# Optimization experiments

Measured on AMD Instinct MI355X. Metric: run time of the kernel, lower is better.

The kernel has to match this reference:

```python
import jax, jax.numpy as jnp
import numpy as np
from jax import lax

B, H, W, C = 8, 128, 128, 256
HEADS, WIN, PRETRAIN = 8, 8, 8
QK_U = C // HEADS            # 32
QK_CH = QK_U * HEADS         # 256
KV_CH = QK_CH + C            # 512
BLOCK = WIN // 2             # key block size at half resolution
HALO = WIN                   # halo window (halo_window//2) at half resolution
PAD = (HALO - BLOCK) // 2    # halo overlap pad at half resolution


def _win_part(x, heads):
    b, h, w, c = x.shape
    u = c // heads
    x = x.reshape(b, h // WIN, WIN, w // WIN, WIN, heads, u)
    x = x.transpose(0, 1, 3, 5, 2, 4, 6)
    return x.reshape(b, (h // WIN) * (w // WIN), heads, WIN * WIN, u)


def _halo_part(x):
    # overlapping halo blocks: [b,hh,wh,c] -> [b, nw, HALO*HALO, c]
    b, h, w, c = x.shape
    xp = jnp.pad(x, ((0, 0), (PAD, PAD), (PAD, PAD), (0, 0)))
    hb, wb = h // BLOCK, w // BLOCK
    ih = jnp.arange(hb)[:, None] * BLOCK + jnp.arange(HALO)[None, :]
    iw = jnp.arange(wb)[:, None] * BLOCK + jnp.arange(HALO)[None, :]
    t = xp[:, ih][:, :, :, iw]            # [b, hb, HALO, wb, HALO, c]
    t = t.transpose(0, 1, 3, 2, 4, 5)
    return t.reshape(b, hb * wb, HALO * HALO, c)


def _halo_part_fused(x, heads):
    t = _halo_part(x)
    b, nw, l, c = t.shape
    u = c // heads
    return t.reshape(b, nw, l, heads, u).transpose(0, 1, 3, 2, 4)


def _l2n(x):
    # tf.math.l2_normalize with epsilon=1.55e-5
    return x * lax.rsqrt(jnp.maximum(jnp.sum(x * x, -1, keepdims=True), 1.55e-5))


def _rel_bias(cpb_w1, cpb_b1, cpb_w2):
    # Swin-V2 style continuous (log-CPB) relative bias between full-res query
    # window and half-res halo key window.
    qc = jnp.arange(WIN, dtype=jnp.float32)
    kc = (jnp.arange(HALO, dtype=jnp.float32) - PAD) * 2.0 + 0.5  # half-res centers in full-res coords
    r1 = qc[:, None] - kc[None, :]
    rel_y = jnp.broadcast_to(r1[:, None, :, None], (WIN, WIN, HALO, HALO))
    rel_x = jnp.broadcast_to(r1[None, :, None, :], (WIN, WIN, HALO, HALO))
    rel = jnp.stack([rel_y, rel_x], -1).reshape(WIN * WIN, HALO * HALO, 2)
    rel = rel / (PRETRAIN - 1) * 8.0
    rel = jnp.sign(rel) * jnp.log2(jnp.abs(rel) + 1.0) / np.float32(np.log2(8.0))
    hmid = jax.nn.relu(rel @ cpb_w1 + cpb_b1)
    bias = 16.0 * jax.nn.sigmoid(hmid @ cpb_w2)   # [q, k, heads]
    return bias.transpose(2, 0, 1)[None, None]    # [1,1,heads,q,k]


def _pad_mask(dtype):
    # No outer divisible-pad here (H,W divisible), but halo zero-padding at the
    # image border must be masked out (-100 on out-of-image key positions).
    m = jnp.ones((1, H // 2, W // 2, 1), dtype)   # min-pooled validity map (all ones)
    hm = _halo_part(m)                            # [1, nw, HALO*HALO, 1]; border halos -> 0
    return -100.0 * (hm[..., 0] == 0).astype(dtype)[:, :, None, None, :]  # [1,nw,1,1,k]


def reference(inputs, qkv_w, q_bias, v_bias, dw_w, dw_gamma, dw_beta, dw_mean, dw_var, scale, cpb_w1, cpb_b1, cpb_w2, proj_w, proj_b):
    qkv = jnp.einsum('bhwc,cd->bhwd', inputs, qkv_w)
    q, kv = qkv[..., :QK_CH], qkv[..., QK_CH:]
    # depthwise 3x3 stride-2 conv + (inference) batch-norm on K/V path
    kv = lax.conv_general_dilated(kv, dw_w, (2, 2), 'SAME',
                                  dimension_numbers=('NHWC', 'HWIO', 'NHWC'),
                                  feature_group_count=KV_CH)
    kv = (kv - dw_mean) * lax.rsqrt(dw_var + 1e-3) * dw_gamma + dw_beta
    q = q + q_bias
    kv = kv + jnp.concatenate([jnp.zeros_like(q_bias), v_bias])
    qw = _win_part(q, HEADS)                                 # [B,nw,h,64,QK_U]
    k = _halo_part_fused(kv[..., :QK_CH], HEADS)             # [B,nw,h,64,QK_U]
    v = _halo_part_fused(kv[..., QK_CH:], HEADS)             # [B,nw,h,64,V_U]
    logit_scale = jnp.exp(jnp.minimum(scale, np.float32(np.log(100.0))))  # [h,1,1]
    attn = jnp.einsum('bnhqd,bnhkd->bnhqk', _l2n(qw) * logit_scale, _l2n(k))
    attn = attn + _rel_bias(cpb_w1, cpb_b1, cpb_w2) + _pad_mask(attn.dtype)
    attn = jax.nn.softmax(attn, axis=-1)
    out = jnp.einsum('bnhqk,bnhkd->bnhqd', attn, v)
    hb, wb = H // WIN, W // WIN
    out = out.reshape(B, hb, wb, HEADS, WIN, WIN, C // HEADS)
    out = out.transpose(0, 1, 4, 2, 5, 3, 6).reshape(B, H, W, C)
    return jnp.einsum('bhwc,cd->bhwd', out, proj_w) + proj_b


def setup_inputs() -> dict:
    key = jax.random.key(0)
    ks = jax.random.split(key, 16)
    rn = lambda k, s, sc=0.05: jax.random.normal(k, s, jnp.float32) * sc
    return {
        'inputs': jax.random.normal(ks[0], (B, H, W, C), jnp.float32),
        'qkv_w': rn(ks[1], (C, 2 * QK_CH + C)),
        'q_bias': rn(ks[2], (QK_CH,)),
        'v_bias': rn(ks[3], (C,)),
        'dw_w': rn(ks[4], (3, 3, 1, KV_CH)),
        'dw_gamma': 1.0 + rn(ks[5], (KV_CH,)),
        'dw_beta': rn(ks[6], (KV_CH,)),
        'dw_mean': rn(ks[7], (KV_CH,)),
        'dw_var': jax.random.uniform(ks[8], (KV_CH,), jnp.float32, 0.5, 1.5),
        'scale': jnp.full((HEADS, 1, 1), np.log(10.0), jnp.float32),
        'cpb_w1': rn(ks[9], (2, 512), 0.5),
        'cpb_b1': rn(ks[10], (512,), 0.1),
        'cpb_w2': rn(ks[11], (512, HEADS), 0.1),
        'proj_w': rn(ks[12], (C, C)),
        'proj_b': rn(ks[13], (C,)),
    }
```

## Files before the change

kernel.cpp:

```cpp
#include <hip/hip_runtime.h>
#include <stdint.h>


typedef __attribute__((ext_vector_type(8))) short short8;
typedef __attribute__((ext_vector_type(4))) short short4v;
typedef __attribute__((ext_vector_type(4))) float f32x4;

#define VT_PLANE 4624L

__device__ __forceinline__ float bf2f(unsigned short u){
  union { unsigned int i; float f; } x; x.i = ((unsigned int)u)<<16; return x.f;
}
__device__ __forceinline__ unsigned short f2bf(float f){
  union { float f; unsigned int i; } x; x.f = f;
  unsigned int r = x.i + 0x7FFFu + ((x.i>>16)&1u);
  return (unsigned short)(r>>16);
}
__device__ __forceinline__ unsigned int pack_bf_t(float a, float b){
  union { float f; unsigned int u; } x, y; x.f = a; y.f = b;
  return (y.u & 0xFFFF0000u) | (x.u >> 16);
}
__device__ __forceinline__ void gl_lds16(const void* g, void* l){
  __builtin_amdgcn_global_load_lds((const __attribute__((address_space(1))) unsigned int*)g,
                                   (__attribute__((address_space(3))) unsigned int*)l, 16, 0, 0);
}

__global__ __launch_bounds__(256) void cvt_bf16_kernel(const float* __restrict__ in,
                                                       short* __restrict__ out, long n8)
{
  long stride = (long)gridDim.x * 256;
  for (long i = (long)blockIdx.x*256 + threadIdx.x; i < n8; i += stride){
    float4 a = ((const float4*)in)[2*i];
    float4 b = ((const float4*)in)[2*i+1];
    short8 v;
    v[0]=(short)f2bf(a.x); v[1]=(short)f2bf(a.y); v[2]=(short)f2bf(a.z); v[3]=(short)f2bf(a.w);
    v[4]=(short)f2bf(b.x); v[5]=(short)f2bf(b.y); v[6]=(short)f2bf(b.z); v[7]=(short)f2bf(b.w);
    ((short8*)out)[i] = v;
  }
}

__global__ void transpose_w_kernel(const float* __restrict__ w, short* __restrict__ wt,
                                   int K, int N)
{
  int idx = blockIdx.x*256 + threadIdx.x;
  if (idx >= K*N) return;
  int n = idx / K, k = idx - n*K;
  wt[idx] = (short)f2bf(w[(long)k*N + n]);
}

__global__ __launch_bounds__(64) void relbias_kernel(const float* __restrict__ w1,
    const float* __restrict__ b1, const float* __restrict__ w2, float* __restrict__ out)
{
  int q = blockIdx.x;
  int k = threadIdx.x;
  float ry = (float)(q>>3) - (((float)(k>>3) - 2.f)*2.f + 0.5f);
  float rx = (float)(q&7)  - (((float)(k&7)  - 2.f)*2.f + 0.5f);
  ry *= (8.f/7.f); rx *= (8.f/7.f);
  float sy = (ry>0.f)?1.f:((ry<0.f)?-1.f:0.f);
  float sx = (rx>0.f)?1.f:((rx<0.f)?-1.f:0.f);
  ry = sy * log2f(fabsf(ry)+1.f) * (1.f/3.f);
  rx = sx * log2f(fabsf(rx)+1.f) * (1.f/3.f);
  float acc[8] = {0,0,0,0,0,0,0,0};
  for (int j=0;j<512;j++){
    float hm = ry*w1[j] + rx*w1[512+j] + b1[j];
    hm = fmaxf(hm, 0.f);
#pragma unroll
    for (int h=0;h<8;h++) acc[h] += hm * w2[j*8+h];
  }
#pragma unroll
  for (int h=0;h<8;h++)
    out[h*4096 + q*64 + k] = (16.f / (1.f + __expf(-acc[h]))) * 1.4426950408889634f;
}

template<int ND, int OUTMODE, int MTILES>
__global__ __launch_bounds__(256) void gemm_bt_kernel(const short* __restrict__ A,
    const short* __restrict__ Bt, const float* __restrict__ bias,
    short* __restrict__ out_q, short* __restrict__ out_kv, float* __restrict__ out_f)
{
  __shared__ short smem[32768];
  const int tid  = threadIdx.x;
  const int lane = tid & 63;
  const int wid  = tid >> 6;
  const int wr = wid >> 1, wc = wid & 1;
  const int g = lane >> 4, q15 = lane & 15;

  constexpr int NCB = ND / 128;
  constexpr int NSUP_X = (1024 / MTILES) / 8;
  const int bid = blockIdx.x;
  const int xcd = bid & 7;
  const int idx = bid >> 3;
  const int sup = xcd * NSUP_X + idx / NCB;
  const long row0 = (long)sup * (128 * MTILES);
  const int  col0 = (idx % NCB) * 128;

  f32x4 acc[4][4];
#pragma unroll
  for (int m=0;m<4;m++)
#pragma unroll
    for (int n=0;n<4;n++) acc[m][n] = (f32x4){0.f,0.f,0.f,0.f};

  auto stage = [&](int s){
    int buf = s & 1;
    long rowt = row0 + (long)(s >> 2) * 128;
    int kt = (s & 3) * 64;
#pragma unroll
    for (int j = 0; j < 4; j++) {
      int f = j*256 + tid;
      int r = f >> 3, p = f & 7;
      gl_lds16(A + (rowt + r)*256 + kt + ((p ^ (r&7))<<3),
               smem + buf*16384 + ((j*256 + (wid<<6))<<3));
      gl_lds16(Bt + (long)(col0 + r)*256 + kt + ((p ^ (r&7))<<3),
               smem + buf*16384 + 8192 + ((j*256 + (wid<<6))<<3));
    }
  };
  auto compute = [&](int buf){
    const short* As = smem + buf*16384;
    const short* Bs = As + 8192;
#pragma unroll
    for (int ks = 0; ks < 2; ks++) {
      short8 af[4], bfv[4];
#pragma unroll
      for (int m=0;m<4;m++){
        int r = wr*64 + m*16 + q15;
        int gg = ks*4 + g;
        af[m] = *(const short8*)(As + r*64 + ((gg ^ (r&7))<<3));
      }
#pragma unroll
      for (int n=0;n<4;n++){
        int r = wc*64 + n*16 + q15;
        int gg = ks*4 + g;
        bfv[n] = *(const short8*)(Bs + r*64 + ((gg ^ (r&7))<<3));
      }
#pragma unroll
      for (int m=0;m<4;m++)
#pragma unroll
        for (int n=0;n<4;n++)
          acc[m][n] = __builtin_amdgcn_mfma_f32_16x16x32_bf16(af[m], bfv[n], acc[m][n], 0, 0, 0);
    }
  };

  stage(0);
  __syncthreads();

  for (int t = 0; t < MTILES; t++){
#pragma unroll
    for (int k = 0; k < 4; k++){
      int s = t*4 + k;
      if (s + 1 < MTILES*4) stage(s+1);
      compute(s & 1);
      __syncthreads();
    }

    if (OUTMODE == 0) {
      short* sc = smem + 16384;
#pragma unroll
      for (int m=0;m<4;m++){
#pragma unroll
        for (int n=0;n<4;n++){
          int col = wc*64 + n*16 + q15;
          int cg = col >> 3;
          float bv = (col0 + col < 256) ? bias[col0 + col] : 0.f;
#pragma unroll
          for (int rg=0;rg<4;rg++){
            int row = wr*64 + m*16 + g*4 + rg;
            sc[row*128 + ((cg ^ (row&7))<<3) + (col&7)] = (short)f2bf(acc[m][n][rg] + bv);
          }
        }
      }
      __syncthreads();
      {
        int row = tid >> 1, ch = tid & 1;
        long grow = row0 + (long)t*128 + row;
#pragma unroll
        for (int j=0;j<8;j++){
          int cg = ch*8 + j;
          short8 v = *(const short8*)(sc + row*128 + ((cg ^ (row&7))<<3));
          int col = col0 + cg*8;
          if (col0 < 256) *(short8*)(out_q + grow*256 + col)        = v;
          else            *(short8*)(out_kv + grow*512 + (col-256)) = v;
        }
      }
      __syncthreads();
    } else {
      float* fsc = (float*)(smem + 16384);
#pragma unroll
      for (int p=0;p<2;p++){
        if (wr == p){
#pragma unroll
          for (int m=0;m<4;m++){
#pragma unroll
            for (int n=0;n<4;n++){
              int col = wc*64 + n*16 + q15;
              int c4 = col >> 2;
              float bv = bias[col0 + col];
#pragma unroll
              for (int rg=0;rg<4;rg++){
                int rl = m*16 + g*4 + rg;
                fsc[rl*128 + ((c4 ^ (rl&7))<<2) + (col&3)] = acc[m][n][rg] + bv;
              }
            }
          }
        }
        __syncthreads();
        {
          int rl = tid >> 2;
          long grow = row0 + (long)t*128 + p*64 + rl;
#pragma unroll
          for (int j=0;j<8;j++){
            int c4 = (tid&3)*8 + j;
            float4 v = *(const float4*)(fsc + rl*128 + ((c4 ^ (rl&7))<<2));
            *(float4*)(out_f + grow*ND + col0 + c4*4) = v;
          }
        }
        __syncthreads();
      }
    }
#pragma unroll
    for (int m=0;m<4;m++)
#pragma unroll
      for (int n=0;n<4;n++) acc[m][n] = (f32x4){0.f,0.f,0.f,0.f};
  }
}

__global__ __launch_bounds__(256) void dwconv_kernel(const short* __restrict__ kv_buf,
    const float* __restrict__ dw_w, const float* __restrict__ gamma,
    const float* __restrict__ beta, const float* __restrict__ mean,
    const float* __restrict__ var, const float* __restrict__ v_bias,
    short* __restrict__ kv_K, short* __restrict__ v_t)
{
  __shared__ short vls[32][256];

  const int bid = blockIdx.x;
  const int b  = bid >> 7;
  const int rem = bid & 127;
  const int y2 = rem >> 1, xq = rem & 1;
  const int tid = threadIdx.x;
  const int lane = tid & 63, w = tid >> 6;
  const int ch0 = lane * 8;

  float s[8], sh[8];
#pragma unroll
  for (int i=0;i<8;i+=4){
    float4 g4 = *(const float4*)(gamma + ch0 + i);
    float4 v4 = *(const float4*)(var   + ch0 + i);
    float4 m4 = *(const float4*)(mean  + ch0 + i);
    float4 b4 = *(const float4*)(beta  + ch0 + i);
    float gg[4] = {g4.x,g4.y,g4.z,g4.w}, vv[4] = {v4.x,v4.y,v4.z,v4.w};
    float mm[4] = {m4.x,m4.y,m4.z,m4.w}, bb[4] = {b4.x,b4.y,b4.z,b4.w};
#pragma unroll
    for (int j=0;j<4;j++){
      float sv = gg[j] * rsqrtf(vv[j] + 1e-3f);
      s[i+j]  = sv;
      sh[i+j] = bb[j] - mm[j]*sv;
    }
  }
  if (ch0 >= 256){
    float4 vb0 = *(const float4*)(v_bias + ch0 - 256);
    float4 vb1 = *(const float4*)(v_bias + ch0 - 252);
    sh[0]+=vb0.x; sh[1]+=vb0.y; sh[2]+=vb0.z; sh[3]+=vb0.w;
    sh[4]+=vb1.x; sh[5]+=vb1.y; sh[6]+=vb1.z; sh[7]+=vb1.w;
  }

  float wv[9][8];
#pragma unroll
  for (int t=0;t<9;t++){
    float4 w0 = *(const float4*)(dw_w + t*512 + ch0);
    float4 w1 = *(const float4*)(dw_w + t*512 + ch0 + 4);
    wv[t][0]=w0.x; wv[t][1]=w0.y; wv[t][2]=w0.z; wv[t][3]=w0.w;
    wv[t][4]=w1.x; wv[t][5]=w1.y; wv[t][6]=w1.z; wv[t][7]=w1.w;
  }

  const int y0 = y2*2;
  const bool vy2 = (y0 + 2) < 128;
  const short* r0 = kv_buf + (((long)b*128 + y0)*128)*512 + ch0;
  const short* r1 = r0 + 128*512;
  const short* r2 = r1 + 128*512;
  const short8 zero8 = {0,0,0,0,0,0,0,0};

  const int x2base = xq*32 + w*8;
  const int xs = x2base*2;

  auto ld = [&](const short* r, int x, bool vy)->short8 {
    if (vy && x < 128) return *(const short8*)(r + (long)x*512);
    return zero8;
  };

  short8 L0 = ld(r0, xs, true), L1 = ld(r1, xs, true), L2 = ld(r2, xs, vy2);

#pragma unroll
  for (int i=0;i<8;i++){
    const int x2 = x2base + i;
    const int xm = xs + 2*i + 1, xr = xs + 2*i + 2;
    short8 M0 = ld(r0, xm, true), M1 = ld(r1, xm, true), M2 = ld(r2, xm, vy2);
    short8 R0 = ld(r0, xr, true), R1 = ld(r1, xr, true), R2 = ld(r2, xr, vy2);

    float acc[8];
#pragma unroll
    for (int c=0;c<8;c++) acc[c] = 0.f;
#pragma unroll
    for (int c=0;c<8;c++){
      acc[c] += bf2f((unsigned short)L0[c]) * wv[0][c];
      acc[c] += bf2f((unsigned short)M0[c]) * wv[1][c];
      acc[c] += bf2f((unsigned short)R0[c]) * wv[2][c];
      acc[c] += bf2f((unsigned short)L1[c]) * wv[3][c];
      acc[c] += bf2f((unsigned short)M1[c]) * wv[4][c];
      acc[c] += bf2f((unsigned short)R1[c]) * wv[5][c];
      acc[c] += bf2f((unsigned short)L2[c]) * wv[6][c];
      acc[c] += bf2f((unsigned short)M2[c]) * wv[7][c];
      acc[c] += bf2f((unsigned short)R2[c]) * wv[8][c];
    }
    short8 o;
#pragma unroll
    for (int c=0;c<8;c++) o[c] = (short)f2bf(acc[c]*s[c] + sh[c]);

    if (ch0 < 256) {
      *(short8*)(kv_K + ((long)((b*64+y2)*64 + x2))*256 + ch0) = o;
    } else {
      *(short8*)(&vls[w*8 + i][ch0 - 256]) = o;
    }
    L0 = R0; L1 = R1; L2 = R2;
  }

  __syncthreads();
  {
    const int cc = tid, hh = cc >> 5, d0 = cc & 31;
    long base = ((long)((b*8+hh)*32 + d0))*VT_PLANE + (long)(y2+2)*68 + xq*32 + 2;
#pragma unroll
    for (int j=0;j<16;j++){
      short2 pr;
      pr.x = vls[2*j][cc];
      pr.y = vls[2*j+1][cc];
      *(short2*)(v_t + base + 2*j) = pr;
    }
  }
}

__global__ __launch_bounds__(256) void halo_attn_kernel(const short* __restrict__ q_buf,
    const short* __restrict__ kv_K, const short* __restrict__ v_t,
    const float* __restrict__ relb, const float* __restrict__ scale,
    short* __restrict__ attn_out)
{
  __shared__ short ps[4][4096];

  const int bid = blockIdx.x;
  const int b = bid >> 8, wno = bid & 255;
  const int bi = wno >> 4, bj = wno & 15;
  const int tid = threadIdx.x;
  const int w = tid >> 6, lane = tid & 63;
  const int g = lane >> 4, q15 = lane & 15;
  short* myps = &ps[w][0];
  const short8 zero8 = {0,0,0,0,0,0,0,0};

  long kbase[4]; bool kval[4];
#pragma unroll
  for (int m=0;m<4;m++){
    int key = m*16 + q15;
    int yy = bi*4-2 + (key>>3), xx = bj*4-2 + (key&7);
    kval[m] = (yy>=0 && yy<64 && xx>=0 && xx<64);
    kbase[m] = ((long)((b*64+yy)*64+xx))*256 + g*8;
  }
  float mkv[4][4];
#pragma unroll
  for (int m=0;m<4;m++)
#pragma unroll
    for (int r=0;r<4;r++){
      int key = m*16 + g*4 + r;
      int yy = bi*4-2+(key>>3), xx = bj*4-2+(key&7);
      mkv[m][r] = (yy>=0&&yy<64&&xx>=0&&xx<64) ? 0.f : -30000.f;
    }
  long qpix[4];
#pragma unroll
  for (int n=0;n<4;n++){
    int q = n*16+q15;
    qpix[n] = ((long)((b*128+bi*8+(q>>3))*128 + bj*8+(q&7)))*256;
  }
  int voff[2];
#pragma unroll
  for (int ks=0;ks<2;ks++) voff[ks] = (bi*4+ks*4+g)*68 + bj*4;

  for (int hi=0; hi<2; hi++){
    const int h = w + hi*4;
    const float lsc = __expf(fminf(scale[h], 4.6051702f)) * 1.4426950408889634f;

    short8 va[2][2];
#pragma unroll
    for (int dblk=0;dblk<2;dblk++){
      long pl = ((long)((b*8+h)*32 + dblk*16 + q15))*VT_PLANE;
#pragma unroll
      for (int ks=0;ks<2;ks++)
        va[dblk][ks] = *(const short8*)(v_t + pl + voff[ks]);
    }

    short8 af[4]; float rkk[4];
#pragma unroll
    for (int m=0;m<4;m++){
      af[m] = kval[m] ? *(const short8*)(kv_K + kbase[m] + h*32) : zero8;
      float ss = 0.f;
#pragma unroll
      for (int e=0;e<8;e++){ float f = bf2f((unsigned short)af[m][e]); ss += f*f; }
      ss += __shfl_xor(ss, 16);
      ss += __shfl_xor(ss, 32);
      rkk[m] = rsqrtf(fmaxf(ss, 1.55e-5f));
    }
    short8 bfv[4]; float rq[4];
#pragma unroll
    for (int n=0;n<4;n++){
      bfv[n] = *(const short8*)(q_buf + qpix[n] + h*32 + g*8);
      float ss = 0.f;
#pragma unroll
      for (int e=0;e<8;e++){ float f = bf2f((unsigned short)bfv[n][e]); ss += f*f; }
      ss += __shfl_xor(ss, 16);
      ss += __shfl_xor(ss, 32);
      rq[n] = rsqrtf(fmaxf(ss, 1.55e-5f)) * lsc;
    }
    float rk[4][4];
#pragma unroll
    for (int m=0;m<4;m++)
#pragma unroll
      for (int r=0;r<4;r++)
        rk[m][r] = __shfl(rkk[m], ((lane>>4)<<2) + r);

    f32x4 sc[4][4];
#pragma unroll
    for (int m=0;m<4;m++)
#pragma unroll
      for (int n=0;n<4;n++)
        sc[m][n] = __builtin_amdgcn_mfma_f32_16x16x32_bf16(af[m], bfv[n],
                       (f32x4){0.f,0.f,0.f,0.f}, 0, 0, 0);

    float mx[4] = {-3e38f,-3e38f,-3e38f,-3e38f};
#pragma unroll
    for (int m=0;m<4;m++){
#pragma unroll
      for (int n=0;n<4;n++){
        f32x4 rb = *(const f32x4*)(relb + h*4096 + (n*16+q15)*64 + m*16 + g*4);
#pragma unroll
        for (int r=0;r<4;r++){
          float v = sc[m][n][r] * (rk[m][r]*rq[n]) + rb[r] + mkv[m][r];
          sc[m][n][r] = v;
          mx[n] = fmaxf(mx[n], v);
        }
      }
    }
#pragma unroll
    for (int n=0;n<4;n++){
      mx[n] = fmaxf(mx[n], __shfl_xor(mx[n], 16));
      mx[n] = fmaxf(mx[n], __shfl_xor(mx[n], 32));
    }
    float sm[4] = {0.f,0.f,0.f,0.f};
#pragma unroll
    for (int m=0;m<4;m++)
#pragma unroll
      for (int n=0;n<4;n++)
#pragma unroll
        for (int r=0;r<4;r++){
          float e = exp2f(sc[m][n][r] - mx[n]);
          sc[m][n][r] = e;
          sm[n] += e;
        }
    float sminv[4];
#pragma unroll
    for (int n=0;n<4;n++){
      sm[n] += __shfl_xor(sm[n], 16);
      sm[n] += __shfl_xor(sm[n], 32);
      sminv[n] = 1.f / sm[n];
    }

#pragma unroll
    for (int n=0;n<4;n++){
      int row = n*16 + q15;
#pragma unroll
      for (int m=0;m<4;m++){
        uint2 pk;
        pk.x = pack_bf_t(sc[m][n][0], sc[m][n][1]);
        pk.y = pack_bf_t(sc[m][n][2], sc[m][n][3]);
        int kc = (m*2 + (g>>1)) ^ (row & 7);
        *(uint2*)(myps + row*64 + kc*8 + ((g&1)<<2)) = pk;
      }
    }
    asm volatile("s_waitcnt lgkmcnt(0)" ::: "memory");

    f32x4 oc[2][4];
#pragma unroll
    for (int dblk=0;dblk<2;dblk++)
#pragma unroll
      for (int n=0;n<4;n++) oc[dblk][n] = (f32x4){0.f,0.f,0.f,0.f};
#pragma unroll
    for (int ks=0;ks<2;ks++){
#pragma unroll
      for (int n=0;n<4;n++){
        int row = n*16 + q15;
        short8 pb = *(const short8*)(myps + row*64 + (((ks*4+g) ^ (row&7))<<3));
#pragma unroll
        for (int dblk=0;dblk<2;dblk++)
          oc[dblk][n] = __builtin_amdgcn_mfma_f32_16x16x32_bf16(va[dblk][ks], pb, oc[dblk][n], 0, 0, 0);
      }
    }

#pragma unroll
    for (int dblk=0;dblk<2;dblk++){
#pragma unroll
      for (int n=0;n<4;n++){
        uint2 pk;
        pk.x = pack_bf_t(oc[dblk][n][0]*sminv[n], oc[dblk][n][1]*sminv[n]);
        pk.y = pack_bf_t(oc[dblk][n][2]*sminv[n], oc[dblk][n][3]*sminv[n]);
        *(uint2*)(attn_out + qpix[n] + h*32 + dblk*16 + g*4) = pk;
      }
    }
  }
}

extern "C" void kernel_launch(void* const* d_in, const int* in_sizes, int n_in,
                              void* d_out, int out_size, void* d_ws, size_t ws_size,
                              hipStream_t stream)
{
  (void)in_sizes; (void)n_in; (void)out_size; (void)ws_size;
  const float* inputs = (const float*)d_in[0];
  const float* qkv_w  = (const float*)d_in[1];
  const float* q_bias = (const float*)d_in[2];
  const float* v_bias = (const float*)d_in[3];
  const float* dw_w   = (const float*)d_in[4];
  const float* dw_g   = (const float*)d_in[5];
  const float* dw_b   = (const float*)d_in[6];
  const float* dw_m   = (const float*)d_in[7];
  const float* dw_v   = (const float*)d_in[8];
  const float* scale  = (const float*)d_in[9];
  const float* cpb_w1 = (const float*)d_in[10];
  const float* cpb_b1 = (const float*)d_in[11];
  const float* cpb_w2 = (const float*)d_in[12];
  const float* proj_w = (const float*)d_in[13];
  const float* proj_b = (const float*)d_in[14];

  char* ws = (char*)d_ws;
  short* q_buf    = (short*)(ws);
  short* kv_buf   = (short*)(ws + 67108864L);
  short* kv_K     = (short*)(ws + 201326592L);
  short* v_t      = (short*)(ws + 218103808L);
  short* attn_buf = (short*)(ws + 237043712L);
  short* qkvw_t   = (short*)(ws + 304152576L);
  short* projw_t  = (short*)(ws + 304939008L);
  float* relb     = (float*)(ws + 305070080L);

  short* a_bf = attn_buf;

  cvt_bf16_kernel<<<2048, 256, 0, stream>>>(inputs, a_bf, 4194304L);
  transpose_w_kernel<<<768, 256, 0, stream>>>(qkv_w, qkvw_t, 256, 768);
  transpose_w_kernel<<<256, 256, 0, stream>>>(proj_w, projw_t, 256, 256);
  relbias_kernel<<<64, 64, 0, stream>>>(cpb_w1, cpb_b1, cpb_w2, relb);

  gemm_bt_kernel<768, 0, 4><<<1536, 256, 0, stream>>>(
      a_bf, qkvw_t, q_bias, q_buf, kv_buf, nullptr);

  dwconv_kernel<<<1024, 256, 0, stream>>>(kv_buf, dw_w, dw_g, dw_b, dw_m, dw_v, v_bias,
                                          kv_K, v_t);

  halo_attn_kernel<<<2048, 256, 0, stream>>>(q_buf, kv_K, v_t, relb, scale, attn_buf);

  gemm_bt_kernel<256, 1, 4><<<512, 256, 0, stream>>>(
      attn_buf, projw_t, proj_b, nullptr, nullptr, (float*)d_out);
}
```

Baseline: 426.7 us.

## Keep weight tile resident in LDS and stream A fragments directly from global

```diff
diff --git a/kernel.cpp b/kernel.cpp
--- a/kernel.cpp
+++ b/kernel.cpp
@@ -15,6 +15,9 @@
   union { float f; unsigned int i; } x; x.f = f;
   unsigned int r = x.i + 0x7FFFu + ((x.i>>16)&1u);
   return (unsigned short)(r>>16);
+}
+__device__ __forceinline__ unsigned int pack_bf_r(float a, float b){
+  return (unsigned int)f2bf(a) | ((unsigned int)f2bf(b) << 16);
 }
 __device__ __forceinline__ unsigned int pack_bf_t(float a, float b){
   union { float f; unsigned int u; } x, y; x.f = a; y.f = b;
@@ -90,135 +93,89 @@
   const int xcd = bid & 7;
   const int idx = bid >> 3;
   const int sup = xcd * NSUP_X + idx / NCB;
-  const long row0 = (long)sup * (128 * MTILES);
-  const int  col0 = (idx % NCB) * 128;
-
-  f32x4 acc[4][4];
-#pragma unroll
-  for (int m=0;m<4;m++)
-#pragma unroll
-    for (int n=0;n<4;n++) acc[m][n] = (f32x4){0.f,0.f,0.f,0.f};
-
-  auto stage = [&](int s){
-    int buf = s & 1;
-    long rowt = row0 + (long)(s >> 2) * 128;
-    int kt = (s & 3) * 64;
-#pragma unroll
-    for (int j = 0; j < 4; j++) {
-      int f = j*256 + tid;
-      int r = f >> 3, p = f & 7;
-      gl_lds16(A + (rowt + r)*256 + kt + ((p ^ (r&7))<<3),
-               smem + buf*16384 + ((j*256 + (wid<<6))<<3));
-      gl_lds16(Bt + (long)(col0 + r)*256 + kt + ((p ^ (r&7))<<3),
-               smem + buf*16384 + 8192 + ((j*256 + (wid<<6))<<3));
-    }
-  };
-  auto compute = [&](int buf){
-    const short* As = smem + buf*16384;
-    const short* Bs = As + 8192;
-#pragma unroll
-    for (int ks = 0; ks < 2; ks++) {
-      short8 af[4], bfv[4];
-#pragma unroll
-      for (int m=0;m<4;m++){
-        int r = wr*64 + m*16 + q15;
-        int gg = ks*4 + g;
-        af[m] = *(const short8*)(As + r*64 + ((gg ^ (r&7))<<3));
-      }
-#pragma unroll
-      for (int n=0;n<4;n++){
-        int r = wc*64 + n*16 + q15;
-        int gg = ks*4 + g;
-        bfv[n] = *(const short8*)(Bs + r*64 + ((gg ^ (r&7))<<3));
-      }
-#pragma unroll
-      for (int m=0;m<4;m++)
-#pragma unroll
-        for (int n=0;n<4;n++)
-          acc[m][n] = __builtin_amdgcn_mfma_f32_16x16x32_bf16(af[m], bfv[n], acc[m][n], 0, 0, 0);
-    }
-  };
-
-  stage(0);
+  const int col0 = (idx % NCB) * 128;
+
+#pragma unroll
+  for (int j = 0; j < 16; j++) {
+    int f = j*256 + tid;
+    int r = f >> 5, c = f & 31;
+    gl_lds16(Bt + (long)(col0 + r)*256 + ((c ^ (r&7))<<3),
+             smem + ((j*256 + (wid<<6))<<3));
+  }
   __syncthreads();
 
+  float4 bv[4];
+#pragma unroll
+  for (int nB=0;nB<4;nB++){
+    int cb = col0 + wc*64 + nB*16 + g*4;
+    if (OUTMODE == 1 || cb < 256) bv[nB] = *(const float4*)(bias + cb);
+    else                          bv[nB] = (float4){0.f,0.f,0.f,0.f};
+  }
+
   for (int t = 0; t < MTILES; t++){
-#pragma unroll
-    for (int k = 0; k < 4; k++){
-      int s = t*4 + k;
-      if (s + 1 < MTILES*4) stage(s+1);
-      compute(s & 1);
-      __syncthreads();
-    }
-
-    if (OUTMODE == 0) {
-      short* sc = smem + 16384;
-#pragma unroll
-      for (int m=0;m<4;m++){
-#pragma unroll
-        for (int n=0;n<4;n++){
-          int col = wc*64 + n*16 + q15;
-          int cg = col >> 3;
-          float bv = (col0 + col < 256) ? bias[col0 + col] : 0.f;
-#pragma unroll
-          for (int rg=0;rg<4;rg++){
-            int row = wr*64 + m*16 + g*4 + rg;
-            sc[row*128 + ((cg ^ (row&7))<<3) + (col&7)] = (short)f2bf(acc[m][n][rg] + bv);
-          }
+    const long rowt = ((long)sup*MTILES + t)*128;
+    const short* Ab = A + (rowt + wr*64 + q15)*256 + g*8;
+
+    f32x4 acc[4][4];
+#pragma unroll
+    for (int mB=0;mB<4;mB++)
+#pragma unroll
+      for (int nB=0;nB<4;nB++) acc[mB][nB] = (f32x4){0.f,0.f,0.f,0.f};
+
+#pragma unroll
+    for (int half = 0; half < 2; half++){
+      short8 af[4][4];
+#pragma unroll
+      for (int mB=0;mB<4;mB++)
+#pragma unroll
+        for (int ksl=0;ksl<4;ksl++)
+          af[mB][ksl] = *(const short8*)(Ab + mB*16*256 + (half*4+ksl)*32);
+#pragma unroll
+      for (int ksl=0;ksl<4;ksl++){
+        const int ks = half*4 + ksl;
+        short8 bf_[4];
+#pragma unroll
+        for (int nB=0;nB<4;nB++){
+          int r = wc*64 + nB*16 + q15;
+          int c = (ks*4 + g) ^ (r&7);
+          bf_[nB] = *(const short8*)(smem + r*256 + c*8);
         }
-      }
-      __syncthreads();
-      {
-        int row = tid >> 1, ch = tid & 1;
-        long grow = row0 + (long)t*128 + row;
-#pragma unroll
-        for (int j=0;j<8;j++){
-          int cg = ch*8 + j;
-          short8 v = *(const short8*)(sc + row*128 + ((cg ^ (row&7))<<3));
-          int col = col0 + cg*8;
-          if (col0 < 256) *(short8*)(out_q + grow*256 + col)        = v;
-          else            *(short8*)(out_kv + grow*512 + (col-256)) = v;
+#pragma unroll
+        for (int mB=0;mB<4;mB++)
+#pragma unroll
+          for (int nB=0;nB<4;nB++)
+            acc[mB][nB] = __builtin_amdgcn_mfma_f32_16x16x32_bf16(bf_[nB], af[mB][ksl], acc[mB][nB], 0, 0, 0);
+      }
+    }
+
+    if (OUTMODE == 0){
+#pragma unroll
+      for (int mB=0;mB<4;mB++){
+        long row = rowt + wr*64 + mB*16 + q15;
+#pragma unroll
+        for (int nB=0;nB<4;nB++){
+          int col = col0 + wc*64 + nB*16 + g*4;
+          uint2 pk;
+          pk.x = pack_bf_r(acc[mB][nB][0]+bv[nB].x, acc[mB][nB][1]+bv[nB].y);
+          pk.y = pack_bf_r(acc[mB][nB][2]+bv[nB].z, acc[mB][nB][3]+bv[nB].w);
+          if (col0 < 256) *(uint2*)(out_q + row*256 + col)        = pk;
+          else            *(uint2*)(out_kv + row*512 + (col-256)) = pk;
         }
       }
-      __syncthreads();
     } else {
-      float* fsc = (float*)(smem + 16384);
-#pragma unroll
-      for (int p=0;p<2;p++){
-        if (wr == p){
-#pragma unroll
-          for (int m=0;m<4;m++){
-#pragma unroll
-            for (int n=0;n<4;n++){
-              int col = wc*64 + n*16 + q15;
-              int c4 = col >> 2;
-              float bv = bias[col0 + col];
-#pragma unroll
-              for (int rg=0;rg<4;rg++){
-                int rl = m*16 + g*4 + rg;
-                fsc[rl*128 + ((c4 ^ (rl&7))<<2) + (col&3)] = acc[m][n][rg] + bv;
-              }
-            }
-          }
+#pragma unroll
+      for (int mB=0;mB<4;mB++){
+        long row = rowt + wr*64 + mB*16 + q15;
+#pragma unroll
+        for (int nB=0;nB<4;nB++){
+          int col = col0 + wc*64 + nB*16 + g*4;
+          float4 o;
+          o.x = acc[mB][nB][0]+bv[nB].x; o.y = acc[mB][nB][1]+bv[nB].y;
+          o.z = acc[mB][nB][2]+bv[nB].z; o.w = acc[mB][nB][3]+bv[nB].w;
+          *(float4*)(out_f + row*ND + col) = o;
         }
-        __syncthreads();
-        {
-          int rl = tid >> 2;
-          long grow = row0 + (long)t*128 + p*64 + rl;
-#pragma unroll
-          for (int j=0;j<8;j++){
-            int c4 = (tid&3)*8 + j;
-            float4 v = *(const float4*)(fsc + rl*128 + ((c4 ^ (rl&7))<<2));
-            *(float4*)(out_f + grow*ND + col0 + c4*4) = v;
-          }
-        }
-        __syncthreads();
-      }
-    }
-#pragma unroll
-    for (int m=0;m<4;m++)
-#pragma unroll
-      for (int n=0;n<4;n++) acc[m][n] = (f32x4){0.f,0.f,0.f,0.f};
+      }
+    }
   }
 }
 
```

New measurement: 486.5 us. +14.0%, slower.

## Restructure GEMM to one tile per block with triple-buffered 32-wide K stages

Applied to the files above, without the earlier changes.

```diff
diff --git a/kernel.cpp b/kernel.cpp
--- a/kernel.cpp
+++ b/kernel.cpp
@@ -72,12 +72,12 @@
     out[h*4096 + q*64 + k] = (16.f / (1.f + __expf(-acc[h]))) * 1.4426950408889634f;
 }
 
-template<int ND, int OUTMODE, int MTILES>
+template<int ND, int OUTMODE>
 __global__ __launch_bounds__(256) void gemm_bt_kernel(const short* __restrict__ A,
     const short* __restrict__ Bt, const float* __restrict__ bias,
     short* __restrict__ out_q, short* __restrict__ out_kv, float* __restrict__ out_f)
 {
-  __shared__ short smem[32768];
+  __shared__ short smem[24576];
   const int tid  = threadIdx.x;
   const int lane = tid & 63;
   const int wid  = tid >> 6;
@@ -85,12 +85,10 @@
   const int g = lane >> 4, q15 = lane & 15;
 
   constexpr int NCB = ND / 128;
-  constexpr int NSUP_X = (1024 / MTILES) / 8;
   const int bid = blockIdx.x;
   const int xcd = bid & 7;
   const int idx = bid >> 3;
-  const int sup = xcd * NSUP_X + idx / NCB;
-  const long row0 = (long)sup * (128 * MTILES);
+  const long row0 = (long)(xcd * 128 + idx / NCB) * 128;
   const int  col0 = (idx % NCB) * 128;
 
   f32x4 acc[4][4];
@@ -100,125 +98,113 @@
     for (int n=0;n<4;n++) acc[m][n] = (f32x4){0.f,0.f,0.f,0.f};
 
   auto stage = [&](int s){
-    int buf = s & 1;
-    long rowt = row0 + (long)(s >> 2) * 128;
-    int kt = (s & 3) * 64;
-#pragma unroll
-    for (int j = 0; j < 4; j++) {
+    int buf = s % 3;
+    int kt = s * 32;
+#pragma unroll
+    for (int j = 0; j < 2; j++) {
       int f = j*256 + tid;
-      int r = f >> 3, p = f & 7;
-      gl_lds16(A + (rowt + r)*256 + kt + ((p ^ (r&7))<<3),
-               smem + buf*16384 + ((j*256 + (wid<<6))<<3));
-      gl_lds16(Bt + (long)(col0 + r)*256 + kt + ((p ^ (r&7))<<3),
-               smem + buf*16384 + 8192 + ((j*256 + (wid<<6))<<3));
+      int r = f >> 2, c = f & 3;
+      int cs = c ^ ((r>>1)&3);
+      gl_lds16(A + (row0 + r)*256 + kt + (cs<<3),
+               smem + buf*8192 + ((j*256 + (wid<<6))<<3));
+      gl_lds16(Bt + (long)(col0 + r)*256 + kt + (cs<<3),
+               smem + buf*8192 + 4096 + ((j*256 + (wid<<6))<<3));
     }
   };
-  auto compute = [&](int buf){
-    const short* As = smem + buf*16384;
-    const short* Bs = As + 8192;
-#pragma unroll
-    for (int ks = 0; ks < 2; ks++) {
-      short8 af[4], bfv[4];
-#pragma unroll
-      for (int m=0;m<4;m++){
-        int r = wr*64 + m*16 + q15;
-        int gg = ks*4 + g;
-        af[m] = *(const short8*)(As + r*64 + ((gg ^ (r&7))<<3));
-      }
+  auto compute = [&](int s){
+    const short* As = smem + (s%3)*8192;
+    const short* Bs = As + 4096;
+    short8 af[4], bfv[4];
+#pragma unroll
+    for (int m=0;m<4;m++){
+      int r = wr*64 + m*16 + q15;
+      af[m] = *(const short8*)(As + (r<<5) + ((g ^ ((r>>1)&3))<<3));
+    }
+#pragma unroll
+    for (int n=0;n<4;n++){
+      int r = wc*64 + n*16 + q15;
+      bfv[n] = *(const short8*)(Bs + (r<<5) + ((g ^ ((r>>1)&3))<<3));
+    }
+#pragma unroll
+    for (int m=0;m<4;m++)
+#pragma unroll
+      for (int n=0;n<4;n++)
+        acc[m][n] = __builtin_amdgcn_mfma_f32_16x16x32_bf16(af[m], bfv[n], acc[m][n], 0, 0, 0);
+  };
+
+  stage(0);
+  stage(1);
+#pragma unroll
+  for (int t = 0; t < 8; t++){
+    if (t < 7) asm volatile("s_waitcnt vmcnt(4) lgkmcnt(0)" ::: "memory");
+    else       asm volatile("s_waitcnt vmcnt(0) lgkmcnt(0)" ::: "memory");
+    asm volatile("s_barrier" ::: "memory");
+    if (t + 2 < 8) stage(t + 2);
+    compute(t);
+  }
+  asm volatile("s_waitcnt lgkmcnt(0)" ::: "memory");
+  asm volatile("s_barrier" ::: "memory");
+
+  if (OUTMODE == 0) {
+    short* sc = smem;
+#pragma unroll
+    for (int m=0;m<4;m++){
 #pragma unroll
       for (int n=0;n<4;n++){
-        int r = wc*64 + n*16 + q15;
-        int gg = ks*4 + g;
-        bfv[n] = *(const short8*)(Bs + r*64 + ((gg ^ (r&7))<<3));
-      }
-#pragma unroll
-      for (int m=0;m<4;m++)
-#pragma unroll
-        for (int n=0;n<4;n++)
-          acc[m][n] = __builtin_amdgcn_mfma_f32_16x16x32_bf16(af[m], bfv[n], acc[m][n], 0, 0, 0);
-    }
-  };
-
-  stage(0);
-  __syncthreads();
-
-  for (int t = 0; t < MTILES; t++){
-#pragma unroll
-    for (int k = 0; k < 4; k++){
-      int s = t*4 + k;
-      if (s + 1 < MTILES*4) stage(s+1);
-      compute(s & 1);
-      __syncthreads();
-    }
-
-    if (OUTMODE == 0) {
-      short* sc = smem + 16384;
-#pragma unroll
-      for (int m=0;m<4;m++){
-#pragma unroll
-        for (int n=0;n<4;n++){
-          int col = wc*64 + n*16 + q15;
-          int cg = col >> 3;
-          float bv = (col0 + col < 256) ? bias[col0 + col] : 0.f;
-#pragma unroll
-          for (int rg=0;rg<4;rg++){
-            int row = wr*64 + m*16 + g*4 + rg;
-            sc[row*128 + ((cg ^ (row&7))<<3) + (col&7)] = (short)f2bf(acc[m][n][rg] + bv);
-          }
+        int col = wc*64 + n*16 + q15;
+        int cg = col >> 3;
+        float bv = (col0 + col < 256) ? bias[col0 + col] : 0.f;
+#pragma unroll
+        for (int rg=0;rg<4;rg++){
+          int row = wr*64 + m*16 + g*4 + rg;
+          sc[row*128 + ((cg ^ (row&7))<<3) + (col&7)] = (short)f2bf(acc[m][n][rg] + bv);
         }
       }
-      __syncthreads();
-      {
-        int row = tid >> 1, ch = tid & 1;
-        long grow = row0 + (long)t*128 + row;
-#pragma unroll
-        for (int j=0;j<8;j++){
-          int cg = ch*8 + j;
-          short8 v = *(const short8*)(sc + row*128 + ((cg ^ (row&7))<<3));
-          int col = col0 + cg*8;
-          if (col0 < 256) *(short8*)(out_q + grow*256 + col)        = v;
-          else            *(short8*)(out_kv + grow*512 + (col-256)) = v;
-        }
-      }
-      __syncthreads();
-    } else {
-      float* fsc = (float*)(smem + 16384);
-#pragma unroll
-      for (int p=0;p<2;p++){
-        if (wr == p){
-#pragma unroll
-          for (int m=0;m<4;m++){
-#pragma unroll
-            for (int n=0;n<4;n++){
-              int col = wc*64 + n*16 + q15;
-              int c4 = col >> 2;
-              float bv = bias[col0 + col];
-#pragma unroll
-              for (int rg=0;rg<4;rg++){
-                int rl = m*16 + g*4 + rg;
-                fsc[rl*128 + ((c4 ^ (rl&7))<<2) + (col&3)] = acc[m][n][rg] + bv;
-              }
+    }
+    __syncthreads();
+    int row = tid >> 1, ch = tid & 1;
+    long grow = row0 + row;
+#pragma unroll
+    for (int j=0;j<8;j++){
+      int cg = ch*8 + j;
+      short8 v = *(const short8*)(sc + row*128 + ((cg ^ (row&7))<<3));
+      int col = col0 + cg*8;
+      if (col0 < 256) *(short8*)(out_q + grow*256 + col)        = v;
+      else            *(short8*)(out_kv + grow*512 + (col-256)) = v;
+    }
+  } else {
+    float* fsc = (float*)smem;
+#pragma unroll
+    for (int p=0;p<2;p++){
+      if (wr == p){
+#pragma unroll
+        for (int m=0;m<4;m++){
+#pragma unroll
+          for (int n=0;n<4;n++){
+            int col = wc*64 + n*16 + q15;
+            int c4 = col >> 2;
+            float bv = bias[col0 + col];
+#pragma unroll
+            for (int rg=0;rg<4;rg++){
+              int rl = m*16 + g*4 + rg;
+              fsc[rl*128 + ((c4 ^ (rl&7))<<2) + (col&3)] = acc[m][n][rg] + bv;
             }
           }
         }
-        __syncthreads();
-        {
-          int rl = tid >> 2;
-          long grow = row0 + (long)t*128 + p*64 + rl;
-#pragma unroll
-          for (int j=0;j<8;j++){
-            int c4 = (tid&3)*8 + j;
-            float4 v = *(const float4*)(fsc + rl*128 + ((c4 ^ (rl&7))<<2));
-            *(float4*)(out_f + grow*ND + col0 + c4*4) = v;
-          }
+      }
+      __syncthreads();
+      {
+        int rl = tid >> 2;
+        long grow = row0 + p*64 + rl;
+#pragma unroll
+        for (int j=0;j<8;j++){
+          int c4 = (tid&3)*8 + j;
+          float4 v = *(const float4*)(fsc + rl*128 + ((c4 ^ (rl&7))<<2));
+          *(float4*)(out_f + grow*ND + col0 + c4*4) = v;
         }
-        __syncthreads();
-      }
-    }
-#pragma unroll
-    for (int m=0;m<4;m++)
-#pragma unroll
-      for (int n=0;n<4;n++) acc[m][n] = (f32x4){0.f,0.f,0.f,0.f};
+      }
+      __syncthreads();
+    }
   }
 }
 
@@ -548,7 +534,7 @@
   transpose_w_kernel<<<256, 256, 0, stream>>>(proj_w, projw_t, 256, 256);
   relbias_kernel<<<64, 64, 0, stream>>>(cpb_w1, cpb_b1, cpb_w2, relb);
 
-  gemm_bt_kernel<768, 0, 4><<<1536, 256, 0, stream>>>(
+  gemm_bt_kernel<768, 0><<<6144, 256, 0, stream>>>(
       a_bf, qkvw_t, q_bias, q_buf, kv_buf, nullptr);
 
   dwconv_kernel<<<1024, 256, 0, stream>>>(kv_buf, dw_w, dw_g, dw_b, dw_m, dw_v, v_bias,
@@ -556,6 +542,6 @@
 
   halo_attn_kernel<<<2048, 256, 0, stream>>>(q_buf, kv_K, v_t, relb, scale, attn_buf);
 
-  gemm_bt_kernel<256, 1, 4><<<512, 256, 0, stream>>>(
+  gemm_bt_kernel<256, 1><<<2048, 256, 0, stream>>>(
       attn_buf, projw_t, proj_b, nullptr, nullptr, (float*)d_out);
 }
```

Result: faster. 408.1 us (-4.4%).
